# Optimization experiments

Hardware: AMD Instinct MI355X
Metric: run time of the kernel (lower is better)

## Reference

```python
import jax, jax.numpy as jnp
import numpy as np
from jax import lax

B, N, D = 256, 257, 768   # batch, 1+num_patches, token dim
K = 8                     # top-k concepts per image
V = 10000                 # codebook size
KMEANS_ITERS = 4
BETA_EMA = 0.99


def _l2norm(x, eps=1e-12):
    return x / jnp.maximum(jnp.linalg.norm(x, axis=-1, keepdims=True), eps)


def setup_inputs() -> dict:
    key = jax.random.key(0)
    k1, k2, k3 = jax.random.split(key, 3)
    tokens = jax.random.normal(k1, (B, N, D), dtype=jnp.float32)
    visual_concepts = jax.random.normal(k2, (V, 2, D), dtype=jnp.float32)
    topk_indices = jax.random.randint(k3, (B, K), 0, V)
    return {"tokens": tokens, "visual_concepts": visual_concepts, "topk_indices": topk_indices}


def reference(tokens, visual_concepts, topk_indices):
    # gather per-image codebook entries: [b, k, 2, d]
    vc_g = _l2norm(visual_concepts[topk_indices])
    tp = tokens[:, 1:]  # drop CLS -> [b, n, d]

    def step(centroids, _):
        sim = jnp.einsum('bnd,bkcd->bnkc', tp, centroids)          # [b,n,k,2]
        assign = jnp.argmax(sim, axis=-1).astype(tp.dtype)          # [b,n,k] in {0,1}
        c1 = jnp.einsum('bnd,bnk->bkd', tp, assign)
        c0 = jnp.einsum('bnd,bnk->bkd', tp, 1.0 - assign)
        centroids = _l2norm(jnp.stack([c0, c1], axis=2))            # [b,k,2,d]
        return centroids, assign

    centroids, assigns = lax.scan(step, vc_g, None, length=KMEANS_ITERS)
    assignments = assigns[-1]  # torch returns the last iteration's assignments

    # NOTE: in the torch code `centroids` aliases the gathered `visual_concepts`
    # and is mutated in-place, so beta*visual_concepts + (1-beta)*centroids == centroids.
    concepts_ema = BETA_EMA * centroids + (1.0 - BETA_EMA) * centroids

    # torch scatter_reduce_ with index shape (b*k, 1, 1) only scatters src[:, 0, 0]
    # into visual_concepts[idx, 0, 0] with reduce='sum' (include_self=True).
    src = concepts_ema.reshape(-1, 2, D)
    idx = topk_indices.reshape(-1)
    vc_new = visual_concepts.at[idx, 0, 0].add(src[:, 0, 0])
    vc_new = _l2norm(vc_new)
    return assignments, vc_new
```

## Files before the change

### kernel.cpp

```cpp
#include <hip/hip_runtime.h>
#include <hip/hip_bf16.h>

#define BB 256
#define NN 257
#define NT 256
#define DD 768
#define KC 8
#define VV 10000
#define ITERS 4

#define CHD 32
#define NCH (DD / CHD)
#define CF4 (CHD / 4)
#define CSTR 193

__device__ __forceinline__ float waveReduceSum(float v) {
#pragma unroll
    for (int off = 32; off > 0; off >>= 1)
        v += __shfl_xor(v, off, 64);
    return v;
}

__device__ __forceinline__ float dot4chain(float4 a, float4 c, float acc) {
    return fmaf(a.w, c.w, fmaf(a.z, c.z, fmaf(a.y, c.y, fmaf(a.x, c.x, acc))));
}

__device__ __forceinline__ void gld16(const float* g, void* lds) {
    __builtin_amdgcn_global_load_lds(
        (const __attribute__((address_space(1))) void*)g,
        (__attribute__((address_space(3))) void*)lds,
        16, 0, 0);
}

__global__ __launch_bounds__(1024, 4) void kmeans_kernel(
    const float* __restrict__ tokens,
    const float* __restrict__ vc,
    const int* __restrict__ topk,
    float* __restrict__ out_assign,
    float* __restrict__ delta)
{
    __shared__ float4 cent4[16 * CSTR];
    __shared__ float4 tbuf4[2 * NT * CF4];
    __shared__ float  tsum[DD];
    __shared__ int sidx[KC];

    float* centf = (float*)cent4;
    float (*c1buf)[DD] = (float (*)[DD])tbuf4;
    float (*maskF)[KC] = (float (*)[KC])((char*)tbuf4 + 24576);

    const int b = blockIdx.x;
    const int t = threadIdx.x;
    const int lane = t & 63;
    const int wave = t >> 6;

    if (t < KC) sidx[t] = topk[b * KC + t];
    __syncthreads();

    {
        const int r = wave;
        const int k = r >> 1, c = r & 1;
        const float* src = vc + ((size_t)sidx[k] * 2 + c) * DD;
        float vals[12];
        float ss = 0.f;
#pragma unroll
        for (int j = 0; j < 12; ++j) {
            vals[j] = src[lane + 64 * j];
            ss = fmaf(vals[j], vals[j], ss);
        }
        ss = waveReduceSum(ss);
        float iv = 1.0f / fmaxf(sqrtf(ss), 1e-12f);
#pragma unroll
        for (int j = 0; j < 12; ++j)
            centf[r * 772 + lane + 64 * j] = vals[j] * iv;
    }
    __syncthreads();

    const float* tpb = tokens + ((size_t)b * NN + 1) * DD;

    const int tok = t & 255;
    const int g   = t >> 8;
    const int s7  = tok & 7;

    const int slotA = wave * 128 + lane;
    const int slotB = slotA + 64;
    const float* gbaseA = tpb + (size_t)(slotA >> 3) * DD + 4 * ((slotA & 7) ^ ((slotA >> 3) & 7));
    const float* gbaseB = tpb + (size_t)(slotB >> 3) * DD + 4 * ((slotB & 7) ^ ((slotB >> 3) & 7));

    for (int it = 0; it < ITERS; ++it) {
        float acc[4] = {0.f, 0.f, 0.f, 0.f};

        gld16(gbaseA, (void*)(tbuf4 + wave * 128));
        gld16(gbaseB, (void*)(tbuf4 + wave * 128 + 64));

        for (int cix = 0; cix < NCH; ++cix) {
            __syncthreads();
            if (cix + 1 < NCH) {
                const int nb = (cix + 1) & 1;
                gld16(gbaseA + (cix + 1) * CHD, (void*)(tbuf4 + nb * 2048 + wave * 128));
                gld16(gbaseB + (cix + 1) * CHD, (void*)(tbuf4 + nb * 2048 + wave * 128 + 64));
            }
            {
                const float4* tb = tbuf4 + (cix & 1) * 2048 + (tok << 3);
                const float4* cr = cent4 + (g * 4) * CSTR + (cix << 3);
#pragma unroll
                for (int j4 = 0; j4 < CF4; ++j4) {
                    float4 a  = tb[j4 ^ s7];
                    float4 c0 = cr[j4];
                    float4 c1 = cr[CSTR + j4];
                    float4 c2 = cr[2 * CSTR + j4];
                    float4 c3 = cr[3 * CSTR + j4];
                    acc[0] = dot4chain(a, c0, acc[0]);
                    acc[1] = dot4chain(a, c1, acc[1]);
                    acc[2] = dot4chain(a, c2, acc[2]);
                    acc[3] = dot4chain(a, c3, acc[3]);
                }
            }
        }

        {
            float2 mf;
            mf.x = (acc[1] > acc[0]) ? 1.f : 0.f;
            mf.y = (acc[3] > acc[2]) ? 1.f : 0.f;
            *(float2*)&maskF[tok][2 * g] = mf;
        }
        __syncthreads();

        if (it == ITERS - 1 && t < NT) {
            const float4* mf4 = (const float4*)&maskF[t][0];
            float4* op = (float4*)(out_assign + ((size_t)b * NT + t) * KC);
            op[0] = mf4[0]; op[1] = mf4[1];
        }

        if (t < DD) {
            const int d = t;
            const float* col = tpb + d;
            const float4* mrow = (const float4*)&maskF[0][0];
            float a0 = 0.f, a1 = 0.f, a2 = 0.f, a3 = 0.f;
            float a4 = 0.f, a5 = 0.f, a6 = 0.f, a7 = 0.f;
            float tr = 0.f;
            for (int n0 = 0; n0 < NT; n0 += 16) {
                float v[16];
#pragma unroll
                for (int u = 0; u < 16; ++u)
                    v[u] = col[(size_t)(n0 + u) * DD];
#pragma unroll
                for (int u = 0; u < 16; ++u) {
                    float4 ma = mrow[2 * (n0 + u)];
                    float4 mb = mrow[2 * (n0 + u) + 1];
                    a0 = fmaf(v[u], ma.x, a0);
                    a1 = fmaf(v[u], ma.y, a1);
                    a2 = fmaf(v[u], ma.z, a2);
                    a3 = fmaf(v[u], ma.w, a3);
                    a4 = fmaf(v[u], mb.x, a4);
                    a5 = fmaf(v[u], mb.y, a5);
                    a6 = fmaf(v[u], mb.z, a6);
                    a7 = fmaf(v[u], mb.w, a7);
                    if (it == 0) tr += v[u];
                }
            }
            c1buf[0][d] = a0; c1buf[1][d] = a1; c1buf[2][d] = a2; c1buf[3][d] = a3;
            c1buf[4][d] = a4; c1buf[5][d] = a5; c1buf[6][d] = a6; c1buf[7][d] = a7;
            if (it == 0) tsum[d] = tr;
        }
        __syncthreads();

        {
            const int k = wave >> 1, cc = wave & 1;
            float vals[12];
            float ss = 0.f;
#pragma unroll
            for (int j = 0; j < 12; ++j) {
                int d = lane + 64 * j;
                float c1v = c1buf[k][d];
                float v = cc ? c1v : (tsum[d] - c1v);
                vals[j] = v;
                ss = fmaf(v, v, ss);
            }
            ss = waveReduceSum(ss);
            float iv = 1.0f / fmaxf(sqrtf(ss), 1e-12f);
#pragma unroll
            for (int j = 0; j < 12; ++j)
                centf[wave * 772 + lane + 64 * j] = vals[j] * iv;
        }
        __syncthreads();
    }

    if (t < KC) {
        atomicAdd(delta + sidx[t], centf[(2 * t) * 772]);
    }
}

__global__ __launch_bounds__(1024) void vcnorm_kernel(
    const float* __restrict__ vc,
    const float* __restrict__ delta,
    float* __restrict__ out)
{
    const int t = threadIdx.x;
    const int lane = t & 63;
    const int wave = t >> 6;
    const int r = blockIdx.x * 16 + wave;
    if (r >= 2 * VV) return;
    const int v = r >> 1;
    const int c = r & 1;
    const float* src = vc + (size_t)r * DD;
    float4 x[3];
#pragma unroll
    for (int j = 0; j < 3; ++j)
        x[j] = *(const float4*)(src + (lane + 64 * j) * 4);
    if (c == 0 && lane == 0) x[0].x += delta[v];
    float ss = 0.f;
#pragma unroll
    for (int j = 0; j < 3; ++j)
        ss += x[j].x * x[j].x + x[j].y * x[j].y + x[j].z * x[j].z + x[j].w * x[j].w;
    ss = waveReduceSum(ss);
    float iv = 1.0f / fmaxf(sqrtf(ss), 1e-12f);
    float* dst = out + (size_t)r * DD;
#pragma unroll
    for (int j = 0; j < 3; ++j) {
        float4 y = make_float4(x[j].x * iv, x[j].y * iv, x[j].z * iv, x[j].w * iv);
        *(float4*)(dst + (lane + 64 * j) * 4) = y;
    }
}

extern "C" void kernel_launch(void* const* d_in, const int* in_sizes, int n_in,
                              void* d_out, int out_size, void* d_ws, size_t ws_size,
                              hipStream_t stream) {
    const float* tokens = (const float*)d_in[0];
    const float* vc     = (const float*)d_in[1];
    const int*   topk   = (const int*)d_in[2];
    float* out          = (float*)d_out;
    float* assignments  = out;
    float* vcnew        = out + (size_t)BB * NT * KC;
    float* delta        = (float*)d_ws;

    hipMemsetAsync(delta, 0, VV * sizeof(float), stream);
    hipLaunchKernelGGL(kmeans_kernel, dim3(BB), dim3(1024), 0, stream,
                       tokens, vc, topk, assignments, delta);
    hipLaunchKernelGGL(vcnorm_kernel, dim3((2 * VV + 15) / 16), dim3(1024), 0, stream,
                       vc, delta, vcnew);
}
```

Before: 681.4 us.

## Triple-buffer token chunks with explicit vmcnt waits and keep token sums in registers

The similarity loop moves from a double-buffered prefetch to a triple-buffered one with a prefetch distance of two. Each step waits with an explicit s_waitcnt vmcnt(2) and a raw barrier instead of __syncthreads, which allows two chunk loads to be in flight during compute. The column-sum phase writes the unnormalized c0/c1 centroids straight into the centroid LDS array and keeps the per-thread token sum in a register, removing the separate c1buf/tsum scratch. This grows LDS use by one chunk buffer, which can lower occupancy, and it depends on the hand-written waitcnt being correct.

```diff
diff --git a/kernel.cpp b/kernel.cpp
--- a/kernel.cpp
+++ b/kernel.cpp
@@ -40,13 +40,11 @@
     float* __restrict__ delta)
 {
     __shared__ float4 cent4[16 * CSTR];
-    __shared__ float4 tbuf4[2 * NT * CF4];
-    __shared__ float  tsum[DD];
+    __shared__ float4 tbuf4[3 * NT * CF4];
     __shared__ int sidx[KC];
 
     float* centf = (float*)cent4;
-    float (*c1buf)[DD] = (float (*)[DD])tbuf4;
-    float (*maskF)[KC] = (float (*)[KC])((char*)tbuf4 + 24576);
+    float (*maskF)[KC] = (float (*)[KC])tbuf4;
 
     const int b = blockIdx.x;
     const int t = threadIdx.x;
@@ -86,21 +84,28 @@
     const float* gbaseA = tpb + (size_t)(slotA >> 3) * DD + 4 * ((slotA & 7) ^ ((slotA >> 3) & 7));
     const float* gbaseB = tpb + (size_t)(slotB >> 3) * DD + 4 * ((slotB & 7) ^ ((slotB >> 3) & 7));
 
+    float tsum_reg = 0.f;
+
     for (int it = 0; it < ITERS; ++it) {
         float acc[4] = {0.f, 0.f, 0.f, 0.f};
 
-        gld16(gbaseA, (void*)(tbuf4 + wave * 128));
-        gld16(gbaseB, (void*)(tbuf4 + wave * 128 + 64));
-
-        for (int cix = 0; cix < NCH; ++cix) {
-            __syncthreads();
-            if (cix + 1 < NCH) {
-                const int nb = (cix + 1) & 1;
-                gld16(gbaseA + (cix + 1) * CHD, (void*)(tbuf4 + nb * 2048 + wave * 128));
-                gld16(gbaseB + (cix + 1) * CHD, (void*)(tbuf4 + nb * 2048 + wave * 128 + 64));
+        gld16(gbaseA,       (void*)(tbuf4 + wave * 128));
+        gld16(gbaseB,       (void*)(tbuf4 + wave * 128 + 64));
+        gld16(gbaseA + CHD, (void*)(tbuf4 + 2048 + wave * 128));
+        gld16(gbaseB + CHD, (void*)(tbuf4 + 2048 + wave * 128 + 64));
+
+#pragma unroll 1
+        for (int cix = 0; cix < NCH - 1; ++cix) {
+            asm volatile("s_waitcnt vmcnt(2)" ::: "memory");
+            __builtin_amdgcn_s_barrier();
+            __builtin_amdgcn_sched_barrier(0);
+            if (cix + 2 < NCH) {
+                const int nb = (cix + 2) % 3;
+                gld16(gbaseA + (cix + 2) * CHD, (void*)(tbuf4 + nb * 2048 + wave * 128));
+                gld16(gbaseB + (cix + 2) * CHD, (void*)(tbuf4 + nb * 2048 + wave * 128 + 64));
             }
             {
-                const float4* tb = tbuf4 + (cix & 1) * 2048 + (tok << 3);
+                const float4* tb = tbuf4 + (cix % 3) * 2048 + (tok << 3);
                 const float4* cr = cent4 + (g * 4) * CSTR + (cix << 3);
 #pragma unroll
                 for (int j4 = 0; j4 < CF4; ++j4) {
@@ -114,6 +119,24 @@
                     acc[2] = dot4chain(a, c2, acc[2]);
                     acc[3] = dot4chain(a, c3, acc[3]);
                 }
+            }
+        }
+        __syncthreads();
+        {
+            const int cix = NCH - 1;
+            const float4* tb = tbuf4 + (cix % 3) * 2048 + (tok << 3);
+            const float4* cr = cent4 + (g * 4) * CSTR + (cix << 3);
+#pragma unroll
+            for (int j4 = 0; j4 < CF4; ++j4) {
+                float4 a  = tb[j4 ^ s7];
+                float4 c0 = cr[j4];
+                float4 c1 = cr[CSTR + j4];
+                float4 c2 = cr[2 * CSTR + j4];
+                float4 c3 = cr[3 * CSTR + j4];
+                acc[0] = dot4chain(a, c0, acc[0]);
+                acc[1] = dot4chain(a, c1, acc[1]);
+                acc[2] = dot4chain(a, c2, acc[2]);
+                acc[3] = dot4chain(a, c3, acc[3]);
             }
         }
 
@@ -158,29 +181,32 @@
                     if (it == 0) tr += v[u];
                 }
             }
-            c1buf[0][d] = a0; c1buf[1][d] = a1; c1buf[2][d] = a2; c1buf[3][d] = a3;
-            c1buf[4][d] = a4; c1buf[5][d] = a5; c1buf[6][d] = a6; c1buf[7][d] = a7;
-            if (it == 0) tsum[d] = tr;
+            if (it == 0) tsum_reg = tr;
+            centf[ 1 * 772 + d] = a0;  centf[ 0 * 772 + d] = tsum_reg - a0;
+            centf[ 3 * 772 + d] = a1;  centf[ 2 * 772 + d] = tsum_reg - a1;
+            centf[ 5 * 772 + d] = a2;  centf[ 4 * 772 + d] = tsum_reg - a2;
+            centf[ 7 * 772 + d] = a3;  centf[ 6 * 772 + d] = tsum_reg - a3;
+            centf[ 9 * 772 + d] = a4;  centf[ 8 * 772 + d] = tsum_reg - a4;
+            centf[11 * 772 + d] = a5;  centf[10 * 772 + d] = tsum_reg - a5;
+            centf[13 * 772 + d] = a6;  centf[12 * 772 + d] = tsum_reg - a6;
+            centf[15 * 772 + d] = a7;  centf[14 * 772 + d] = tsum_reg - a7;
         }
         __syncthreads();
 
         {
-            const int k = wave >> 1, cc = wave & 1;
+            const int r = wave;
             float vals[12];
             float ss = 0.f;
 #pragma unroll
             for (int j = 0; j < 12; ++j) {
-                int d = lane + 64 * j;
-                float c1v = c1buf[k][d];
-                float v = cc ? c1v : (tsum[d] - c1v);
-                vals[j] = v;
-                ss = fmaf(v, v, ss);
+                vals[j] = centf[r * 772 + lane + 64 * j];
+                ss = fmaf(vals[j], vals[j], ss);
             }
             ss = waveReduceSum(ss);
             float iv = 1.0f / fmaxf(sqrtf(ss), 1e-12f);
 #pragma unroll
             for (int j = 0; j < 12; ++j)
-                centf[wave * 772 + lane + 64 * j] = vals[j] * iv;
+                centf[r * 772 + lane + 64 * j] = vals[j] * iv;
         }
         __syncthreads();
     }
```

After: 648.6 us. 4.8% less time.
